# Kernel optimization log

Hardware: AMD Instinct MI355X
Metric: run time of the kernel (lower is better)

## Reference

```python
import jax, jax.numpy as jnp
import numpy as np
from jax import lax
from jax.scipy.linalg import expm

B, T, H, NCLS = 256, 784, 512, 10


def setup_inputs() -> dict:
    key = jax.random.key(0)
    ks = jax.random.split(key, 6)
    inputs = jax.random.normal(ks[0], (B, T), dtype=jnp.float32)
    # faithful to Model: fixed permutation from RandomState(92916)
    permutation = jnp.asarray(np.random.RandomState(92916).permutation(T), dtype=jnp.int64)
    W_skew = jax.random.normal(ks[1], (H, H), dtype=jnp.float32) * 0.05  # free param for skew-symmetric A
    W_in = jax.random.normal(ks[2], (H, 1), dtype=jnp.float32)            # Linear(1, H, bias=False)
    b_mod = jax.random.uniform(ks[3], (H,), dtype=jnp.float32, minval=-0.01, maxval=0.01)  # modrelu bias
    W_lin = jax.random.normal(ks[4], (NCLS, H), dtype=jnp.float32) * 0.05
    b_lin = jax.random.normal(ks[5], (NCLS,), dtype=jnp.float32) * 0.05
    return {"inputs": inputs, "permutation": permutation, "W_skew": W_skew,
            "W_in": W_in, "b_mod": b_mod, "W_lin": W_lin, "b_lin": b_lin}


def reference(inputs, permutation, W_skew, W_in, b_mod, W_lin, b_lin):
    # permuted-pixel input sequence: [B, T]
    x = inputs[:, permutation]
    # expm parametrization of the orthogonal recurrent kernel:
    # A = triu(W,1) - triu(W,1)^T (skew-symmetric), Borth = expm(A) is orthogonal
    Au = jnp.triu(W_skew, 1)
    Borth = expm(Au - Au.T)  # [H, H]
    # precompute all input projections: Linear(1,H) on each scalar pixel -> [T, B, H]
    proj = x.T[:, :, None] * W_in[:, 0][None, None, :]

    def step(h, u):
        pre = u + h @ Borth                                  # [B, H]
        h_new = jnp.sign(pre) * jax.nn.relu(jnp.abs(pre) + b_mod)  # modrelu
        return h_new, None

    h0 = jnp.zeros((inputs.shape[0], W_in.shape[0]), dtype=inputs.dtype)
    hT, _ = lax.scan(step, h0, proj)
    return hT @ W_lin.T + b_lin  # [B, 10]
```

## Files before the change

kernel.cpp:

```cpp
#include <hip/hip_runtime.h>

#define TSTEPS 784
#define BATCH  256
#define HDIM   512
#define NCLS   10
#define NGRP   16
#define WGPG   8

typedef __bf16 bf16x8 __attribute__((ext_vector_type(8)));
typedef float  f32x4  __attribute__((ext_vector_type(4)));
typedef unsigned uint4v __attribute__((ext_vector_type(4)));
typedef unsigned long long u64;
typedef unsigned short u16;

static __device__ __forceinline__ u16 f2bf(float f) {
  unsigned u = __builtin_bit_cast(unsigned, f);
  u += 0x7fffu + ((u >> 16) & 1u);
  return (u16)(u >> 16);
}
static __device__ __forceinline__ float bf2f(unsigned s) {
  unsigned u = s << 16;
  return __builtin_bit_cast(float, u);
}

__global__ __launch_bounds__(256) void gather_xp(const float* __restrict__ in,
                                                 const int* __restrict__ perm,
                                                 float* __restrict__ xp) {
  int t = blockIdx.x;
  int b = threadIdx.x;
  int p = perm[t];
  p = (p < 0) ? 0 : (p >= TSTEPS ? TSTEPS - 1 : p);
  xp[t * BATCH + b] = in[b * TSTEPS + p];
}

__global__ __launch_bounds__(256) void build_X(const float* __restrict__ W,
                                               float* __restrict__ X) {
  int idx = blockIdx.x * 256 + threadIdx.x;
  int i = idx >> 9, j = idx & 511;
  float v = 0.f;
  if (j > i) v = W[i * HDIM + j];
  else if (i > j) v = -W[j * HDIM + i];
  X[idx] = v * 0.03125f;
}

__global__ __launch_bounds__(256) void axpyI(float* __restrict__ P,
                                             const float* __restrict__ X, float coef) {
  int idx = blockIdx.x * 256 + threadIdx.x;
  int i = idx >> 9, j = idx & 511;
  P[idx] = coef * X[idx] + ((i == j) ? 1.f : 0.f);
}

__global__ __launch_bounds__(256) void gemm512(float* __restrict__ C,
                                               const float* __restrict__ A,
                                               const float* __restrict__ B,
                                               float alpha, int addI) {
  __shared__ float As[16][68];
  __shared__ float Bs[16][68];
  const int tx = threadIdx.x, ty = threadIdx.y;
  const int tid = ty * 16 + tx;
  const int ib = blockIdx.y, jb = blockIdx.x;
  const int ra = tid >> 2, ca = (tid & 3) << 2;
  const int rb = tid >> 4, cb = (tid & 15) << 2;
  float acc[4][4] = {};
  for (int kt = 0; kt < HDIM / 16; ++kt) {
    f32x4 av = *(const f32x4*)(A + (ib * 64 + ra) * HDIM + kt * 16 + ca);
    f32x4 bv = *(const f32x4*)(B + (kt * 16 + rb) * HDIM + jb * 64 + cb);
    __syncthreads();
    As[ca + 0][ra] = av[0];
    As[ca + 1][ra] = av[1];
    As[ca + 2][ra] = av[2];
    As[ca + 3][ra] = av[3];
    *(f32x4*)&Bs[rb][cb] = bv;
    __syncthreads();
#pragma unroll
    for (int kk = 0; kk < 16; ++kk) {
      f32x4 a4 = *(const f32x4*)&As[kk][ty << 2];
      f32x4 b4 = *(const f32x4*)&Bs[kk][tx << 2];
#pragma unroll
      for (int u = 0; u < 4; ++u)
#pragma unroll
        for (int v = 0; v < 4; ++v) acc[u][v] = fmaf(a4[u], b4[v], acc[u][v]);
    }
  }
#pragma unroll
  for (int u = 0; u < 4; ++u)
#pragma unroll
    for (int v = 0; v < 4; ++v) {
      int r = ib * 64 + (ty << 2) + u, c = jb * 64 + (tx << 2) + v;
      float val = alpha * acc[u][v];
      if (addI && r == c) val += 1.f;
      C[r * HDIM + c] = val;
    }
}

__global__ __launch_bounds__(256, 1) void rnn_main(
    const float* __restrict__ xp, const float* __restrict__ Borth,
    const float* __restrict__ W_in, const float* __restrict__ b_mod,
    const float* __restrict__ W_lin, const float* __restrict__ b_lin,
    unsigned* __restrict__ h0, unsigned* __restrict__ h1,
    float* __restrict__ out) {
  __shared__ unsigned tile0[8192], tile1[8192];

  const int wg = blockIdx.x;
  const int gb = wg & 15;
  const int cg = wg >> 4;
  const int tid = threadIdx.x;
  const int wave = tid >> 6;
  const int lane = tid & 63;
  const int quad = lane >> 4;
  const int l16 = lane & 15;
  const int colg = (cg << 6) + (wave << 4) + l16;
  const int hbase = (cg << 6) + (wave << 4) + (quad << 2);

  bf16x8 Bfh[16], Bfl[16];
#pragma unroll
  for (int ki = 0; ki < 16; ++ki) {
#pragma unroll
    for (int j = 0; j < 8; ++j) {
      int k = (ki << 5) + (quad << 3) + j;
      float v = Borth[k * HDIM + colg];
      u16 hb = f2bf(v);
      u16 lb = f2bf(v - bf2f(hb));
      Bfh[ki][j] = __builtin_bit_cast(__bf16, hb);
      Bfl[ki][j] = __builtin_bit_cast(__bf16, lb);
    }
  }
  const f32x4 win4 = *(const f32x4*)(W_in + hbase);
  const f32x4 bm4 = *(const f32x4*)(b_mod + hbase);

  const u64 b0 = (u64)(h0 + (gb << 13));
  const u64 b1 = (u64)(h1 + (gb << 13));
  const unsigned vo0 = (unsigned)((tid + 0 * 256) << 4);
  const unsigned vo1 = (unsigned)((tid + 1 * 256) << 4);
  const unsigned vo2 = (unsigned)((tid + 2 * 256) << 4);
  const unsigned vo3 = (unsigned)((tid + 3 * 256) << 4);
  const unsigned vo4 = (unsigned)((tid + 4 * 256) << 4);
  const unsigned vo5 = (unsigned)((tid + 5 * 256) << 4);
  const unsigned vo6 = (unsigned)((tid + 6 * 256) << 4);
  const unsigned vo7 = (unsigned)((tid + 7 * 256) << 4);
  const unsigned soff = (unsigned)(((l16 << 9) + hbase) << 2);
  const unsigned swz = (unsigned)((l16 & 7) << 2);

  for (int t = 0; t < TSTEPS; ++t) {
    const u64 rb = (t & 1) ? b1 : b0;
    const u64 wb = (t & 1) ? b0 : b1;
    const unsigned rtag = (unsigned)((t >> 1) & 1);
    const unsigned wtag = (unsigned)(((t + 1) >> 1) & 1);
    unsigned* const tl = (t & 1) ? tile1 : tile0;

    uint4v q0, q1, q2, q3, q4, q5, q6, q7;
    int spin = 0;
    for (;;) {
      asm volatile(
          "global_load_dwordx4 %[q0], %[v0], %[b] sc1\n\t"
          "global_load_dwordx4 %[q1], %[v1], %[b] sc1\n\t"
          "global_load_dwordx4 %[q2], %[v2], %[b] sc1\n\t"
          "global_load_dwordx4 %[q3], %[v3], %[b] sc1\n\t"
          "global_load_dwordx4 %[q4], %[v4], %[b] sc1\n\t"
          "global_load_dwordx4 %[q5], %[v5], %[b] sc1\n\t"
          "global_load_dwordx4 %[q6], %[v6], %[b] sc1\n\t"
          "global_load_dwordx4 %[q7], %[v7], %[b] sc1\n\t"
          "s_waitcnt vmcnt(0)"
          : [q0] "=&v"(q0), [q1] "=&v"(q1), [q2] "=&v"(q2), [q3] "=&v"(q3),
            [q4] "=&v"(q4), [q5] "=&v"(q5), [q6] "=&v"(q6), [q7] "=&v"(q7)
          : [v0] "v"(vo0), [v1] "v"(vo1), [v2] "v"(vo2), [v3] "v"(vo3),
            [v4] "v"(vo4), [v5] "v"(vo5), [v6] "v"(vo6), [v7] "v"(vo7),
            [b] "s"(rb));
      unsigned bad = 0;
#define TCHK(q) bad |= (q[0] ^ rtag) | (q[1] ^ rtag) | (q[2] ^ rtag) | (q[3] ^ rtag)
      TCHK(q0); TCHK(q1); TCHK(q2); TCHK(q3);
      TCHK(q4); TCHK(q5); TCHK(q6); TCHK(q7);
#undef TCHK
      if (!(bad & 1u)) break;
      __builtin_amdgcn_s_sleep(1);
      if (++spin > (1 << 11)) break;
    }
    __builtin_amdgcn_sched_barrier(0);

#define STG(g, q)                                                      \
  {                                                                    \
    int G = tid + ((g) << 8);                                          \
    int r = G >> 7;                                                    \
    unsigned dc = (unsigned)(G & 127) << 2;                            \
    unsigned phys = ((unsigned)r << 9) | (dc ^ ((unsigned)(r & 7) << 2)); \
    *(uint4v*)(tl + phys) = q;                                         \
  }
    STG(0, q0) STG(1, q1) STG(2, q2) STG(3, q3)
    STG(4, q4) STG(5, q5) STG(6, q6) STG(7, q7)
#undef STG
    __syncthreads();

    f32x4 hh = {0.f, 0.f, 0.f, 0.f};
    f32x4 lh = {0.f, 0.f, 0.f, 0.f};
    f32x4 hl = {0.f, 0.f, 0.f, 0.f};
#pragma unroll
    for (int ki = 0; ki < 16; ++ki) {
      unsigned dc0 = (unsigned)((ki << 5) + (quad << 3));
      unsigned base = (unsigned)l16 << 9;
      unsigned offL = base + (dc0 ^ swz);
      unsigned offH = base + ((dc0 + 4) ^ swz);
      uint4v e0 = *(const uint4v*)(tl + offL);
      uint4v e1 = *(const uint4v*)(tl + offH);
      uint4v ahv, alv;
      ahv[0] = __builtin_amdgcn_perm(e0[1], e0[0], 0x07060302u);
      ahv[1] = __builtin_amdgcn_perm(e0[3], e0[2], 0x07060302u);
      ahv[2] = __builtin_amdgcn_perm(e1[1], e1[0], 0x07060302u);
      ahv[3] = __builtin_amdgcn_perm(e1[3], e1[2], 0x07060302u);
      alv[0] = __builtin_amdgcn_perm(e0[1], e0[0], 0x05040100u);
      alv[1] = __builtin_amdgcn_perm(e0[3], e0[2], 0x05040100u);
      alv[2] = __builtin_amdgcn_perm(e1[1], e1[0], 0x05040100u);
      alv[3] = __builtin_amdgcn_perm(e1[3], e1[2], 0x05040100u);
      bf16x8 ah = __builtin_bit_cast(bf16x8, ahv);
      bf16x8 al = __builtin_bit_cast(bf16x8, alv);
      hh = __builtin_amdgcn_mfma_f32_16x16x32_bf16(Bfh[ki], ah, hh, 0, 0, 0);
      lh = __builtin_amdgcn_mfma_f32_16x16x32_bf16(Bfh[ki], al, lh, 0, 0, 0);
      hl = __builtin_amdgcn_mfma_f32_16x16x32_bf16(Bfl[ki], ah, hl, 0, 0, 0);
    }

    {
      float xs = xp[t * BATCH + (gb << 4) + l16];
      uint4v sv;
#pragma unroll
      for (int r = 0; r < 4; ++r) {
        float pre = hh[r] + lh[r] + hl[r] + xs * win4[r];
        float mm = fmaxf(fabsf(pre) + bm4[r], 0.f);
        float hv = (pre > 0.f) ? mm : ((pre < 0.f) ? -mm : 0.f);
        u16 hbv = f2bf(hv);
        u16 lbv = f2bf(hv - bf2f(hbv));
        sv[r] = ((unsigned)hbv << 16) | (unsigned)((lbv & 0xFFFEu) | wtag);
      }
      asm volatile("global_store_dwordx4 %[o], %[d], %[b] sc1" ::[o] "v"(soff),
                   [d] "v"(sv), [b] "s"(wb));
    }
  }

  if (cg == 0) {
    uint4v q0, q1, q2, q3, q4, q5, q6, q7;
    const unsigned rtag = 0u;
    int spin = 0;
    for (;;) {
      asm volatile(
          "global_load_dwordx4 %[q0], %[v0], %[b] sc1\n\t"
          "global_load_dwordx4 %[q1], %[v1], %[b] sc1\n\t"
          "global_load_dwordx4 %[q2], %[v2], %[b] sc1\n\t"
          "global_load_dwordx4 %[q3], %[v3], %[b] sc1\n\t"
          "global_load_dwordx4 %[q4], %[v4], %[b] sc1\n\t"
          "global_load_dwordx4 %[q5], %[v5], %[b] sc1\n\t"
          "global_load_dwordx4 %[q6], %[v6], %[b] sc1\n\t"
          "global_load_dwordx4 %[q7], %[v7], %[b] sc1\n\t"
          "s_waitcnt vmcnt(0)"
          : [q0] "=&v"(q0), [q1] "=&v"(q1), [q2] "=&v"(q2), [q3] "=&v"(q3),
            [q4] "=&v"(q4), [q5] "=&v"(q5), [q6] "=&v"(q6), [q7] "=&v"(q7)
          : [v0] "v"(vo0), [v1] "v"(vo1), [v2] "v"(vo2), [v3] "v"(vo3),
            [v4] "v"(vo4), [v5] "v"(vo5), [v6] "v"(vo6), [v7] "v"(vo7),
            [b] "s"(b0));
      unsigned bad = 0;
#define TCHK(q) bad |= (q[0] ^ rtag) | (q[1] ^ rtag) | (q[2] ^ rtag) | (q[3] ^ rtag)
      TCHK(q0); TCHK(q1); TCHK(q2); TCHK(q3);
      TCHK(q4); TCHK(q5); TCHK(q6); TCHK(q7);
#undef TCHK
      if (!(bad & 1u)) break;
      __builtin_amdgcn_s_sleep(1);
      if (++spin > (1 << 11)) break;
    }
    __builtin_amdgcn_sched_barrier(0);
#define STG(g, q)                                                      \
  {                                                                    \
    int G = tid + ((g) << 8);                                          \
    int r = G >> 7;                                                    \
    unsigned dc = (unsigned)(G & 127) << 2;                            \
    unsigned phys = ((unsigned)r << 9) | (dc ^ ((unsigned)(r & 7) << 2)); \
    *(uint4v*)(tile0 + phys) = q;                                      \
  }
    STG(0, q0) STG(1, q1) STG(2, q2) STG(3, q3)
    STG(4, q4) STG(5, q5) STG(6, q6) STG(7, q7)
#undef STG
    __syncthreads();
    int row = tid >> 4;
    int cls = tid & 15;
    if (cls < NCLS) {
      float acc = b_lin[cls];
      const float* wl = W_lin + cls * HDIM;
      for (int k = 0; k < HDIM; ++k) {
        unsigned phys = ((unsigned)row << 9) |
                        ((unsigned)k ^ (((unsigned)row & 7) << 2));
        unsigned x = tile0[phys];
        float hv = bf2f(x >> 16) + bf2f(x & 0xFFFFu);
        acc = fmaf(hv, wl[k], acc);
      }
      out[((gb << 4) + row) * NCLS + cls] = acc;
    }
  }
}

extern "C" void kernel_launch(void* const* d_in, const int* in_sizes, int n_in,
                              void* d_out, int out_size, void* d_ws, size_t ws_size,
                              hipStream_t stream) {
  const float* inputs = (const float*)d_in[0];
  const int* perm = (const int*)d_in[1];
  const float* W_skew = (const float*)d_in[2];
  const float* W_in = (const float*)d_in[3];
  const float* b_mod = (const float*)d_in[4];
  const float* W_lin = (const float*)d_in[5];
  const float* b_lin = (const float*)d_in[6];
  float* out = (float*)d_out;

  char* ws = (char*)d_ws;
  unsigned* h0 = (unsigned*)ws;
  unsigned* h1 = h0 + BATCH * HDIM;
  float* xp = (float*)(h1 + BATCH * HDIM);
  float* X = xp + TSTEPS * BATCH;
  float* P = X + HDIM * HDIM;
  float* Q = P + HDIM * HDIM;

  hipMemsetAsync(h0, 0, (size_t)BATCH * HDIM * 4, stream);
  hipMemsetAsync(h1, 0x01, (size_t)BATCH * HDIM * 4, stream);

  gather_xp<<<TSTEPS, 256, 0, stream>>>(inputs, perm, xp);
  build_X<<<(HDIM * HDIM) / 256, 256, 0, stream>>>(W_skew, X);

  axpyI<<<(HDIM * HDIM) / 256, 256, 0, stream>>>(P, X, 1.f / 6.f);
  float* a = P;
  float* b = Q;
  for (int k = 5; k >= 1; --k) {
    gemm512<<<dim3(8, 8), dim3(16, 16), 0, stream>>>(b, X, a, 1.f / (float)k, 1);
    float* tmp = a; a = b; b = tmp;
  }
  for (int i = 0; i < 5; ++i) {
    gemm512<<<dim3(8, 8), dim3(16, 16), 0, stream>>>(b, a, a, 1.f, 0);
    float* tmp = a; a = b; b = tmp;
  }

  rnn_main<<<NGRP * WGPG, 256, 0, stream>>>(xp, a, W_in, b_mod, W_lin, b_lin,
                                            h0, h1, out);
  (void)in_sizes; (void)n_in; (void)out_size; (void)ws_size;
}
```

Measured before the change: 2.994 ms.

## Load hidden state directly into MFMA registers, drop LDS staging and barrier

Each wave now loads exactly the h fragments it needs from global memory straight into registers with per-lane offsets, removing the LDS staging stores, the __syncthreads, and the LDS reads per step. Readiness is checked per k-chunk via wave ballot, so MFMAs on chunks that have arrived proceed while only pending chunks are re-polled. This trades the shared cooperative load for redundant per-wave global loads (each wave fetches the full 16x512 slice) and more VGPRs for the 32 fragment registers.

```diff
diff --git a/kernel.cpp b/kernel.cpp
--- a/kernel.cpp
+++ b/kernel.cpp
@@ -99,7 +99,7 @@
     const float* __restrict__ W_lin, const float* __restrict__ b_lin,
     unsigned* __restrict__ h0, unsigned* __restrict__ h1,
     float* __restrict__ out) {
-  __shared__ unsigned tile0[8192], tile1[8192];
+  __shared__ unsigned tile0[8192];
 
   const int wg = blockIdx.x;
   const int gb = wg & 15;
@@ -130,25 +130,131 @@
 
   const u64 b0 = (u64)(h0 + (gb << 13));
   const u64 b1 = (u64)(h1 + (gb << 13));
-  const unsigned vo0 = (unsigned)((tid + 0 * 256) << 4);
-  const unsigned vo1 = (unsigned)((tid + 1 * 256) << 4);
-  const unsigned vo2 = (unsigned)((tid + 2 * 256) << 4);
-  const unsigned vo3 = (unsigned)((tid + 3 * 256) << 4);
-  const unsigned vo4 = (unsigned)((tid + 4 * 256) << 4);
-  const unsigned vo5 = (unsigned)((tid + 5 * 256) << 4);
-  const unsigned vo6 = (unsigned)((tid + 6 * 256) << 4);
-  const unsigned vo7 = (unsigned)((tid + 7 * 256) << 4);
+  const unsigned rvoff = (unsigned)((l16 << 11) + (quad << 5));
   const unsigned soff = (unsigned)(((l16 << 9) + hbase) << 2);
-  const unsigned swz = (unsigned)((l16 & 7) << 2);
+
+  uint4v q00, q01, q02, q03, q10, q11, q12, q13;
+  uint4v q20, q21, q22, q23, q30, q31, q32, q33;
+  uint4v q40, q41, q42, q43, q50, q51, q52, q53;
+  uint4v q60, q61, q62, q63, q70, q71, q72, q73;
+
+#define ISSUE(c, O0, O1, O2, O3)                                          \
+  asm volatile("global_load_dwordx4 %0, %4, %5 offset:" #O0 " sc1\n\t"    \
+               "global_load_dwordx4 %1, %4, %5 offset:" #O1 " sc1\n\t"    \
+               "global_load_dwordx4 %2, %4, %5 offset:" #O2 " sc1\n\t"    \
+               "global_load_dwordx4 %3, %4, %5 offset:" #O3 " sc1"        \
+               : "=&v"(q##c##0), "=&v"(q##c##1), "=&v"(q##c##2),          \
+                 "=&v"(q##c##3)                                           \
+               : "v"(rvoff), "s"(rb));
+#define ISSUE_ALL                                                         \
+  ISSUE(0, 0, 16, 128, 144)                                               \
+  ISSUE(1, 256, 272, 384, 400)                                            \
+  ISSUE(2, 512, 528, 640, 656)                                            \
+  ISSUE(3, 768, 784, 896, 912)                                            \
+  ISSUE(4, 1024, 1040, 1152, 1168)                                        \
+  ISSUE(5, 1280, 1296, 1408, 1424)                                        \
+  ISSUE(6, 1536, 1552, 1664, 1680)                                        \
+  ISSUE(7, 1792, 1808, 1920, 1936)
+#define REISSUE(c, O0, O1, O2, O3)                                        \
+  if (pend & (1u << c)) { ISSUE(c, O0, O1, O2, O3) }
+#define REISSUE_ALL                                                       \
+  REISSUE(0, 0, 16, 128, 144)                                             \
+  REISSUE(1, 256, 272, 384, 400)                                          \
+  REISSUE(2, 512, 528, 640, 656)                                          \
+  REISSUE(3, 768, 784, 896, 912)                                          \
+  REISSUE(4, 1024, 1040, 1152, 1168)                                      \
+  REISSUE(5, 1280, 1296, 1408, 1424)                                      \
+  REISSUE(6, 1536, 1552, 1664, 1680)                                      \
+  REISSUE(7, 1792, 1808, 1920, 1936)
+
+#define MFMA_HALF(E0, E1, KI)                                             \
+  {                                                                       \
+    uint4v ahv, alv;                                                      \
+    ahv[0] = __builtin_amdgcn_perm(E0[1], E0[0], 0x07060302u);            \
+    ahv[1] = __builtin_amdgcn_perm(E0[3], E0[2], 0x07060302u);            \
+    ahv[2] = __builtin_amdgcn_perm(E1[1], E1[0], 0x07060302u);            \
+    ahv[3] = __builtin_amdgcn_perm(E1[3], E1[2], 0x07060302u);            \
+    alv[0] = __builtin_amdgcn_perm(E0[1], E0[0], 0x05040100u);            \
+    alv[1] = __builtin_amdgcn_perm(E0[3], E0[2], 0x05040100u);            \
+    alv[2] = __builtin_amdgcn_perm(E1[1], E1[0], 0x05040100u);            \
+    alv[3] = __builtin_amdgcn_perm(E1[3], E1[2], 0x05040100u);            \
+    bf16x8 ah = __builtin_bit_cast(bf16x8, ahv);                          \
+    bf16x8 al = __builtin_bit_cast(bf16x8, alv);                          \
+    hh = __builtin_amdgcn_mfma_f32_16x16x32_bf16(Bfh[KI], ah, hh, 0, 0, 0); \
+    lh = __builtin_amdgcn_mfma_f32_16x16x32_bf16(Bfh[KI], al, lh, 0, 0, 0); \
+    hl = __builtin_amdgcn_mfma_f32_16x16x32_bf16(Bfl[KI], ah, hl, 0, 0, 0); \
+  }
+#define PROC(c)                                                           \
+  if (pend & (1u << c)) {                                                 \
+    unsigned orv = (q##c##0[0] ^ rmask) | (q##c##0[1] ^ rmask) |          \
+                   (q##c##0[2] ^ rmask) | (q##c##0[3] ^ rmask) |          \
+                   (q##c##1[0] ^ rmask) | (q##c##1[1] ^ rmask) |          \
+                   (q##c##1[2] ^ rmask) | (q##c##1[3] ^ rmask) |          \
+                   (q##c##2[0] ^ rmask) | (q##c##2[1] ^ rmask) |          \
+                   (q##c##2[2] ^ rmask) | (q##c##2[3] ^ rmask) |          \
+                   (q##c##3[0] ^ rmask) | (q##c##3[1] ^ rmask) |          \
+                   (q##c##3[2] ^ rmask) | (q##c##3[3] ^ rmask);           \
+    if (__ballot((orv & 1u) == 0u) == ~0ull) {                            \
+      MFMA_HALF(q##c##0, q##c##1, 2 * c)                                  \
+      MFMA_HALF(q##c##2, q##c##3, 2 * c + 1)                              \
+      pend &= ~(1u << c);                                                 \
+    }                                                                     \
+  }
 
   for (int t = 0; t < TSTEPS; ++t) {
     const u64 rb = (t & 1) ? b1 : b0;
     const u64 wb = (t & 1) ? b0 : b1;
-    const unsigned rtag = (unsigned)((t >> 1) & 1);
+    const unsigned rmask = ((t >> 1) & 1) ? 0xFFFFFFFFu : 0u;
     const unsigned wtag = (unsigned)(((t + 1) >> 1) & 1);
-    unsigned* const tl = (t & 1) ? tile1 : tile0;
-
-    uint4v q0, q1, q2, q3, q4, q5, q6, q7;
+
+    const float xs = xp[t * BATCH + (gb << 4) + l16];
+
+    f32x4 hh = {0.f, 0.f, 0.f, 0.f};
+    f32x4 lh = {0.f, 0.f, 0.f, 0.f};
+    f32x4 hl = {0.f, 0.f, 0.f, 0.f};
+
+    ISSUE_ALL
+    asm volatile("s_waitcnt vmcnt(0)" ::: "memory");
+    __builtin_amdgcn_sched_barrier(0);
+
+    unsigned pend = 0xffu;
+    int spin = 0;
+    for (;;) {
+      PROC(0) PROC(1) PROC(2) PROC(3) PROC(4) PROC(5) PROC(6) PROC(7)
+      if (!pend) break;
+      if (++spin > (1 << 11)) break;
+      __builtin_amdgcn_s_sleep(1);
+      REISSUE_ALL
+      asm volatile("s_waitcnt vmcnt(0)" ::: "memory");
+      __builtin_amdgcn_sched_barrier(0);
+    }
+
+    {
+      uint4v sv;
+#pragma unroll
+      for (int r = 0; r < 4; ++r) {
+        float pre = hh[r] + lh[r] + hl[r] + xs * win4[r];
+        float mm = fmaxf(fabsf(pre) + bm4[r], 0.f);
+        float hv = (pre > 0.f) ? mm : ((pre < 0.f) ? -mm : 0.f);
+        u16 hbv = f2bf(hv);
+        u16 lbv = f2bf(hv - bf2f(hbv));
+        sv[r] = ((unsigned)hbv << 16) | (unsigned)((lbv & 0xFFFEu) | wtag);
+      }
+      asm volatile("global_store_dwordx4 %[o], %[d], %[b] sc1" ::[o] "v"(soff),
+                   [d] "v"(sv), [b] "s"(wb));
+    }
+  }
+
+  if (cg == 0) {
+    const unsigned vo0 = (unsigned)((tid + 0 * 256) << 4);
+    const unsigned vo1 = (unsigned)((tid + 1 * 256) << 4);
+    const unsigned vo2 = (unsigned)((tid + 2 * 256) << 4);
+    const unsigned vo3 = (unsigned)((tid + 3 * 256) << 4);
+    const unsigned vo4 = (unsigned)((tid + 4 * 256) << 4);
+    const unsigned vo5 = (unsigned)((tid + 5 * 256) << 4);
+    const unsigned vo6 = (unsigned)((tid + 6 * 256) << 4);
+    const unsigned vo7 = (unsigned)((tid + 7 * 256) << 4);
+    uint4v p0, p1, p2, p3, p4, p5, p6, p7;
     int spin = 0;
     for (;;) {
       asm volatile(
@@ -161,103 +267,15 @@
           "global_load_dwordx4 %[q6], %[v6], %[b] sc1\n\t"
           "global_load_dwordx4 %[q7], %[v7], %[b] sc1\n\t"
           "s_waitcnt vmcnt(0)"
-          : [q0] "=&v"(q0), [q1] "=&v"(q1), [q2] "=&v"(q2), [q3] "=&v"(q3),
-            [q4] "=&v"(q4), [q5] "=&v"(q5), [q6] "=&v"(q6), [q7] "=&v"(q7)
-          : [v0] "v"(vo0), [v1] "v"(vo1), [v2] "v"(vo2), [v3] "v"(vo3),
-            [v4] "v"(vo4), [v5] "v"(vo5), [v6] "v"(vo6), [v7] "v"(vo7),
-            [b] "s"(rb));
-      unsigned bad = 0;
-#define TCHK(q) bad |= (q[0] ^ rtag) | (q[1] ^ rtag) | (q[2] ^ rtag) | (q[3] ^ rtag)
-      TCHK(q0); TCHK(q1); TCHK(q2); TCHK(q3);
-      TCHK(q4); TCHK(q5); TCHK(q6); TCHK(q7);
-#undef TCHK
-      if (!(bad & 1u)) break;
-      __builtin_amdgcn_s_sleep(1);
-      if (++spin > (1 << 11)) break;
-    }
-    __builtin_amdgcn_sched_barrier(0);
-
-#define STG(g, q)                                                      \
-  {                                                                    \
-    int G = tid + ((g) << 8);                                          \
-    int r = G >> 7;                                                    \
-    unsigned dc = (unsigned)(G & 127) << 2;                            \
-    unsigned phys = ((unsigned)r << 9) | (dc ^ ((unsigned)(r & 7) << 2)); \
-    *(uint4v*)(tl + phys) = q;                                         \
-  }
-    STG(0, q0) STG(1, q1) STG(2, q2) STG(3, q3)
-    STG(4, q4) STG(5, q5) STG(6, q6) STG(7, q7)
-#undef STG
-    __syncthreads();
-
-    f32x4 hh = {0.f, 0.f, 0.f, 0.f};
-    f32x4 lh = {0.f, 0.f, 0.f, 0.f};
-    f32x4 hl = {0.f, 0.f, 0.f, 0.f};
-#pragma unroll
-    for (int ki = 0; ki < 16; ++ki) {
-      unsigned dc0 = (unsigned)((ki << 5) + (quad << 3));
-      unsigned base = (unsigned)l16 << 9;
-      unsigned offL = base + (dc0 ^ swz);
-      unsigned offH = base + ((dc0 + 4) ^ swz);
-      uint4v e0 = *(const uint4v*)(tl + offL);
-      uint4v e1 = *(const uint4v*)(tl + offH);
-      uint4v ahv, alv;
-      ahv[0] = __builtin_amdgcn_perm(e0[1], e0[0], 0x07060302u);
-      ahv[1] = __builtin_amdgcn_perm(e0[3], e0[2], 0x07060302u);
-      ahv[2] = __builtin_amdgcn_perm(e1[1], e1[0], 0x07060302u);
-      ahv[3] = __builtin_amdgcn_perm(e1[3], e1[2], 0x07060302u);
-      alv[0] = __builtin_amdgcn_perm(e0[1], e0[0], 0x05040100u);
-      alv[1] = __builtin_amdgcn_perm(e0[3], e0[2], 0x05040100u);
-      alv[2] = __builtin_amdgcn_perm(e1[1], e1[0], 0x05040100u);
-      alv[3] = __builtin_amdgcn_perm(e1[3], e1[2], 0x05040100u);
-      bf16x8 ah = __builtin_bit_cast(bf16x8, ahv);
-      bf16x8 al = __builtin_bit_cast(bf16x8, alv);
-      hh = __builtin_amdgcn_mfma_f32_16x16x32_bf16(Bfh[ki], ah, hh, 0, 0, 0);
-      lh = __builtin_amdgcn_mfma_f32_16x16x32_bf16(Bfh[ki], al, lh, 0, 0, 0);
-      hl = __builtin_amdgcn_mfma_f32_16x16x32_bf16(Bfl[ki], ah, hl, 0, 0, 0);
-    }
-
-    {
-      float xs = xp[t * BATCH + (gb << 4) + l16];
-      uint4v sv;
-#pragma unroll
-      for (int r = 0; r < 4; ++r) {
-        float pre = hh[r] + lh[r] + hl[r] + xs * win4[r];
-        float mm = fmaxf(fabsf(pre) + bm4[r], 0.f);
-        float hv = (pre > 0.f) ? mm : ((pre < 0.f) ? -mm : 0.f);
-        u16 hbv = f2bf(hv);
-        u16 lbv = f2bf(hv - bf2f(hbv));
-        sv[r] = ((unsigned)hbv << 16) | (unsigned)((lbv & 0xFFFEu) | wtag);
-      }
-      asm volatile("global_store_dwordx4 %[o], %[d], %[b] sc1" ::[o] "v"(soff),
-                   [d] "v"(sv), [b] "s"(wb));
-    }
-  }
-
-  if (cg == 0) {
-    uint4v q0, q1, q2, q3, q4, q5, q6, q7;
-    const unsigned rtag = 0u;
-    int spin = 0;
-    for (;;) {
-      asm volatile(
-          "global_load_dwordx4 %[q0], %[v0], %[b] sc1\n\t"
-          "global_load_dwordx4 %[q1], %[v1], %[b] sc1\n\t"
-          "global_load_dwordx4 %[q2], %[v2], %[b] sc1\n\t"
-          "global_load_dwordx4 %[q3], %[v3], %[b] sc1\n\t"
-          "global_load_dwordx4 %[q4], %[v4], %[b] sc1\n\t"
-          "global_load_dwordx4 %[q5], %[v5], %[b] sc1\n\t"
-          "global_load_dwordx4 %[q6], %[v6], %[b] sc1\n\t"
-          "global_load_dwordx4 %[q7], %[v7], %[b] sc1\n\t"
-          "s_waitcnt vmcnt(0)"
-          : [q0] "=&v"(q0), [q1] "=&v"(q1), [q2] "=&v"(q2), [q3] "=&v"(q3),
-            [q4] "=&v"(q4), [q5] "=&v"(q5), [q6] "=&v"(q6), [q7] "=&v"(q7)
+          : [q0] "=&v"(p0), [q1] "=&v"(p1), [q2] "=&v"(p2), [q3] "=&v"(p3),
+            [q4] "=&v"(p4), [q5] "=&v"(p5), [q6] "=&v"(p6), [q7] "=&v"(p7)
           : [v0] "v"(vo0), [v1] "v"(vo1), [v2] "v"(vo2), [v3] "v"(vo3),
             [v4] "v"(vo4), [v5] "v"(vo5), [v6] "v"(vo6), [v7] "v"(vo7),
             [b] "s"(b0));
       unsigned bad = 0;
-#define TCHK(q) bad |= (q[0] ^ rtag) | (q[1] ^ rtag) | (q[2] ^ rtag) | (q[3] ^ rtag)
-      TCHK(q0); TCHK(q1); TCHK(q2); TCHK(q3);
-      TCHK(q4); TCHK(q5); TCHK(q6); TCHK(q7);
+#define TCHK(q) bad |= q[0] | q[1] | q[2] | q[3]
+      TCHK(p0); TCHK(p1); TCHK(p2); TCHK(p3);
+      TCHK(p4); TCHK(p5); TCHK(p6); TCHK(p7);
 #undef TCHK
       if (!(bad & 1u)) break;
       __builtin_amdgcn_s_sleep(1);
@@ -272,8 +290,8 @@
     unsigned phys = ((unsigned)r << 9) | (dc ^ ((unsigned)(r & 7) << 2)); \
     *(uint4v*)(tile0 + phys) = q;                                      \
   }
-    STG(0, q0) STG(1, q1) STG(2, q2) STG(3, q3)
-    STG(4, q4) STG(5, q5) STG(6, q6) STG(7, q7)
+    STG(0, p0) STG(1, p1) STG(2, p2) STG(3, p3)
+    STG(4, p4) STG(5, p5) STG(6, p6) STG(7, p7)
 #undef STG
     __syncthreads();
     int row = tid >> 4;
```

After: 5.918 ms. +97.7%, slower.

## Prefetch next-step hidden state loads and re-poll only stale groups

Applied to the files above, without the earlier changes.

Issues the eight tagged global loads for the next timestep right after storing the current hidden state, so the poll latency overlaps the store and loop overhead. The spin loop now re-loads only the groups whose tag check failed, and the s_sleep backoff is removed. The x projection load is also hoisted before the wait. The early loads are more likely to see stale data and need retries, and spinning without sleep adds memory traffic.

```diff
diff --git a/kernel.cpp b/kernel.cpp
--- a/kernel.cpp
+++ b/kernel.cpp
@@ -141,53 +141,67 @@
   const unsigned soff = (unsigned)(((l16 << 9) + hbase) << 2);
   const unsigned swz = (unsigned)((l16 & 7) << 2);
 
+  uint4v q0, q1, q2, q3, q4, q5, q6, q7;
+
+#define ISSUE_ALL(B)                                                        \
+  asm volatile("global_load_dwordx4 %[q0], %[v0], %[b] sc1\n\t"             \
+               "global_load_dwordx4 %[q1], %[v1], %[b] sc1\n\t"             \
+               "global_load_dwordx4 %[q2], %[v2], %[b] sc1\n\t"             \
+               "global_load_dwordx4 %[q3], %[v3], %[b] sc1\n\t"             \
+               "global_load_dwordx4 %[q4], %[v4], %[b] sc1\n\t"             \
+               "global_load_dwordx4 %[q5], %[v5], %[b] sc1\n\t"             \
+               "global_load_dwordx4 %[q6], %[v6], %[b] sc1\n\t"             \
+               "global_load_dwordx4 %[q7], %[v7], %[b] sc1"                 \
+               : [q0] "=&v"(q0), [q1] "=&v"(q1), [q2] "=&v"(q2),            \
+                 [q3] "=&v"(q3), [q4] "=&v"(q4), [q5] "=&v"(q5),            \
+                 [q6] "=&v"(q6), [q7] "=&v"(q7)                             \
+               : [v0] "v"(vo0), [v1] "v"(vo1), [v2] "v"(vo2),               \
+                 [v3] "v"(vo3), [v4] "v"(vo4), [v5] "v"(vo5),               \
+                 [v6] "v"(vo6), [v7] "v"(vo7), [b] "s"(B));
+#define CHKG(g)                                                             \
+  if (pend & (1u << g)) {                                                   \
+    unsigned orv = (q##g[0] ^ rmask) | (q##g[1] ^ rmask) |                  \
+                   (q##g[2] ^ rmask) | (q##g[3] ^ rmask);                   \
+    if (!(orv & 1u)) pend &= ~(1u << g);                                    \
+  }
+#define RLDG(g, B)                                                          \
+  if (pend & (1u << g))                                                     \
+    asm volatile("global_load_dwordx4 %0, %1, %2 sc1"                       \
+                 : "=&v"(q##g) : "v"(vo##g), "s"(B));
+#define STG(g, q, TL)                                                       \
+  {                                                                         \
+    int G = tid + ((g) << 8);                                               \
+    int r = G >> 7;                                                         \
+    unsigned dc = (unsigned)(G & 127) << 2;                                 \
+    unsigned phys = ((unsigned)r << 9) | (dc ^ ((unsigned)(r & 7) << 2));   \
+    *(uint4v*)(TL + phys) = q;                                              \
+  }
+
+  ISSUE_ALL(b0)
+
   for (int t = 0; t < TSTEPS; ++t) {
     const u64 rb = (t & 1) ? b1 : b0;
     const u64 wb = (t & 1) ? b0 : b1;
-    const unsigned rtag = (unsigned)((t >> 1) & 1);
+    const unsigned rmask = ((t >> 1) & 1) ? 0xFFFFFFFFu : 0u;
     const unsigned wtag = (unsigned)(((t + 1) >> 1) & 1);
     unsigned* const tl = (t & 1) ? tile1 : tile0;
 
-    uint4v q0, q1, q2, q3, q4, q5, q6, q7;
+    const float xs = xp[t * BATCH + (gb << 4) + l16];
+
+    unsigned pend = 0xffu;
     int spin = 0;
     for (;;) {
-      asm volatile(
-          "global_load_dwordx4 %[q0], %[v0], %[b] sc1\n\t"
-          "global_load_dwordx4 %[q1], %[v1], %[b] sc1\n\t"
-          "global_load_dwordx4 %[q2], %[v2], %[b] sc1\n\t"
-          "global_load_dwordx4 %[q3], %[v3], %[b] sc1\n\t"
-          "global_load_dwordx4 %[q4], %[v4], %[b] sc1\n\t"
-          "global_load_dwordx4 %[q5], %[v5], %[b] sc1\n\t"
-          "global_load_dwordx4 %[q6], %[v6], %[b] sc1\n\t"
-          "global_load_dwordx4 %[q7], %[v7], %[b] sc1\n\t"
-          "s_waitcnt vmcnt(0)"
-          : [q0] "=&v"(q0), [q1] "=&v"(q1), [q2] "=&v"(q2), [q3] "=&v"(q3),
-            [q4] "=&v"(q4), [q5] "=&v"(q5), [q6] "=&v"(q6), [q7] "=&v"(q7)
-          : [v0] "v"(vo0), [v1] "v"(vo1), [v2] "v"(vo2), [v3] "v"(vo3),
-            [v4] "v"(vo4), [v5] "v"(vo5), [v6] "v"(vo6), [v7] "v"(vo7),
-            [b] "s"(rb));
-      unsigned bad = 0;
-#define TCHK(q) bad |= (q[0] ^ rtag) | (q[1] ^ rtag) | (q[2] ^ rtag) | (q[3] ^ rtag)
-      TCHK(q0); TCHK(q1); TCHK(q2); TCHK(q3);
-      TCHK(q4); TCHK(q5); TCHK(q6); TCHK(q7);
-#undef TCHK
-      if (!(bad & 1u)) break;
-      __builtin_amdgcn_s_sleep(1);
+      asm volatile("s_waitcnt vmcnt(0)" ::: "memory");
+      __builtin_amdgcn_sched_barrier(0);
+      CHKG(0) CHKG(1) CHKG(2) CHKG(3) CHKG(4) CHKG(5) CHKG(6) CHKG(7)
+      if (!pend) break;
       if (++spin > (1 << 11)) break;
-    }
-    __builtin_amdgcn_sched_barrier(0);
-
-#define STG(g, q)                                                      \
-  {                                                                    \
-    int G = tid + ((g) << 8);                                          \
-    int r = G >> 7;                                                    \
-    unsigned dc = (unsigned)(G & 127) << 2;                            \
-    unsigned phys = ((unsigned)r << 9) | (dc ^ ((unsigned)(r & 7) << 2)); \
-    *(uint4v*)(tl + phys) = q;                                         \
-  }
-    STG(0, q0) STG(1, q1) STG(2, q2) STG(3, q3)
-    STG(4, q4) STG(5, q5) STG(6, q6) STG(7, q7)
-#undef STG
+      RLDG(0, rb) RLDG(1, rb) RLDG(2, rb) RLDG(3, rb)
+      RLDG(4, rb) RLDG(5, rb) RLDG(6, rb) RLDG(7, rb)
+    }
+
+    STG(0, q0, tl) STG(1, q1, tl) STG(2, q2, tl) STG(3, q3, tl)
+    STG(4, q4, tl) STG(5, q5, tl) STG(6, q6, tl) STG(7, q7, tl)
     __syncthreads();
 
     f32x4 hh = {0.f, 0.f, 0.f, 0.f};
@@ -218,7 +232,6 @@
     }
 
     {
-      float xs = xp[t * BATCH + (gb << 4) + l16];
       uint4v sv;
 #pragma unroll
       for (int r = 0; r < 4; ++r) {
@@ -232,49 +245,25 @@
       asm volatile("global_store_dwordx4 %[o], %[d], %[b] sc1" ::[o] "v"(soff),
                    [d] "v"(sv), [b] "s"(wb));
     }
+
+    ISSUE_ALL(wb)
   }
 
   if (cg == 0) {
-    uint4v q0, q1, q2, q3, q4, q5, q6, q7;
-    const unsigned rtag = 0u;
+    const unsigned rmask = 0u;
+    unsigned pend = 0xffu;
     int spin = 0;
     for (;;) {
-      asm volatile(
-          "global_load_dwordx4 %[q0], %[v0], %[b] sc1\n\t"
-          "global_load_dwordx4 %[q1], %[v1], %[b] sc1\n\t"
-          "global_load_dwordx4 %[q2], %[v2], %[b] sc1\n\t"
-          "global_load_dwordx4 %[q3], %[v3], %[b] sc1\n\t"
-          "global_load_dwordx4 %[q4], %[v4], %[b] sc1\n\t"
-          "global_load_dwordx4 %[q5], %[v5], %[b] sc1\n\t"
-          "global_load_dwordx4 %[q6], %[v6], %[b] sc1\n\t"
-          "global_load_dwordx4 %[q7], %[v7], %[b] sc1\n\t"
-          "s_waitcnt vmcnt(0)"
-          : [q0] "=&v"(q0), [q1] "=&v"(q1), [q2] "=&v"(q2), [q3] "=&v"(q3),
-            [q4] "=&v"(q4), [q5] "=&v"(q5), [q6] "=&v"(q6), [q7] "=&v"(q7)
-          : [v0] "v"(vo0), [v1] "v"(vo1), [v2] "v"(vo2), [v3] "v"(vo3),
-            [v4] "v"(vo4), [v5] "v"(vo5), [v6] "v"(vo6), [v7] "v"(vo7),
-            [b] "s"(b0));
-      unsigned bad = 0;
-#define TCHK(q) bad |= (q[0] ^ rtag) | (q[1] ^ rtag) | (q[2] ^ rtag) | (q[3] ^ rtag)
-      TCHK(q0); TCHK(q1); TCHK(q2); TCHK(q3);
-      TCHK(q4); TCHK(q5); TCHK(q6); TCHK(q7);
-#undef TCHK
-      if (!(bad & 1u)) break;
-      __builtin_amdgcn_s_sleep(1);
+      asm volatile("s_waitcnt vmcnt(0)" ::: "memory");
+      __builtin_amdgcn_sched_barrier(0);
+      CHKG(0) CHKG(1) CHKG(2) CHKG(3) CHKG(4) CHKG(5) CHKG(6) CHKG(7)
+      if (!pend) break;
       if (++spin > (1 << 11)) break;
-    }
-    __builtin_amdgcn_sched_barrier(0);
-#define STG(g, q)                                                      \
-  {                                                                    \
-    int G = tid + ((g) << 8);                                          \
-    int r = G >> 7;                                                    \
-    unsigned dc = (unsigned)(G & 127) << 2;                            \
-    unsigned phys = ((unsigned)r << 9) | (dc ^ ((unsigned)(r & 7) << 2)); \
-    *(uint4v*)(tile0 + phys) = q;                                      \
-  }
-    STG(0, q0) STG(1, q1) STG(2, q2) STG(3, q3)
-    STG(4, q4) STG(5, q5) STG(6, q6) STG(7, q7)
-#undef STG
+      RLDG(0, b0) RLDG(1, b0) RLDG(2, b0) RLDG(3, b0)
+      RLDG(4, b0) RLDG(5, b0) RLDG(6, b0) RLDG(7, b0)
+    }
+    STG(0, q0, tile0) STG(1, q1, tile0) STG(2, q2, tile0) STG(3, q3, tile0)
+    STG(4, q4, tile0) STG(5, q5, tile0) STG(6, q6, tile0) STG(7, q7, tile0)
     __syncthreads();
     int row = tid >> 4;
     int cls = tid & 15;
```

Measured after the change: 4.352 ms. 45.4% more time.
